# Kernel optimization log

Hardware: AMD Instinct MI355X
Metric: run time of the kernel (lower is better)

## Reference

```python
import jax, jax.numpy as jnp
import numpy as np

B, T, H, NH = 4, 1024, 1024, 16
HS = H // NH
FF = 4 * H
EPS = 1e-5


def setup_inputs() -> dict:
    key = jax.random.key(0)
    ks = jax.random.split(key, 12)
    s = 0.02
    inp = {
        "x": jax.random.normal(ks[0], (B, T, H), jnp.float32),
        # attention projections, stored as [in, out] so y = x @ W + b
        "Wq": jax.random.normal(ks[1], (H, H), jnp.float32) * s,
        "bq": jnp.zeros((H,), jnp.float32),
        "Wk": jax.random.normal(ks[2], (H, H), jnp.float32) * s,
        "bk": jnp.zeros((H,), jnp.float32),
        "Wv": jax.random.normal(ks[3], (H, H), jnp.float32) * s,
        "bv": jnp.zeros((H,), jnp.float32),
        "Wo": jax.random.normal(ks[4], (H, H), jnp.float32) * s,
        "bo": jnp.zeros((H,), jnp.float32),
        # layernorms
        "ln1_w": jnp.ones((H,), jnp.float32),
        "ln1_b": jnp.zeros((H,), jnp.float32),
        "ln2_w": jnp.ones((H,), jnp.float32),
        "ln2_b": jnp.zeros((H,), jnp.float32),
        # MLP
        "Wfc": jax.random.normal(ks[5], (H, FF), jnp.float32) * s,
        "bfc": jnp.zeros((FF,), jnp.float32),
        "Wpr": jax.random.normal(ks[6], (FF, H), jnp.float32) * s,
        "bpr": jnp.zeros((H,), jnp.float32),
    }
    return inp


def _layernorm(x, w, b):
    mu = jnp.mean(x, axis=-1, keepdims=True)
    var = jnp.mean(jnp.square(x - mu), axis=-1, keepdims=True)
    return (x - mu) * jax.lax.rsqrt(var + EPS) * w + b


def _rope(x):
    # x: [B, nh, T, hs]; interleaved-pair RoPE, base 10000
    half = HS // 2
    inv_freq = 1.0 / (10000.0 ** (jnp.arange(half, dtype=jnp.float32) / half))
    ang = jnp.arange(T, dtype=jnp.float32)[:, None] * inv_freq[None, :]  # [T, half]
    cos, sin = jnp.cos(ang), jnp.sin(ang)
    xr = x.reshape(*x.shape[:-1], half, 2)
    x0, x1 = xr[..., 0], xr[..., 1]
    r0 = x0 * cos - x1 * sin
    r1 = x0 * sin + x1 * cos
    return jnp.stack([r0, r1], axis=-1).reshape(x.shape)


def _block(x, Wq, bq, Wk, bk, Wv, bv, Wo, bo, ln1_w, ln1_b, ln2_w, ln2_b, Wfc, bfc, Wpr, bpr):
    # --- attention sub-block ---
    h1 = _layernorm(x, ln1_w, ln1_b)
    q = (h1 @ Wq + bq).reshape(B, T, NH, HS).transpose(0, 2, 1, 3)  # [B,nh,T,hs]
    k = (h1 @ Wk + bk).reshape(B, T, NH, HS).transpose(0, 2, 1, 3)
    v = (h1 @ Wv + bv).reshape(B, T, NH, HS).transpose(0, 2, 1, 3)
    q, k = _rope(q), _rope(k)
    scores = jnp.einsum('bhqd,bhkd->bhqk', q, k) / jnp.sqrt(jnp.float32(HS))
    attn = jax.nn.softmax(scores, axis=-1)
    # NOTE: original applies the causal mask AFTER softmax (multiplicative, no renorm)
    causal = jnp.tril(jnp.ones((T, T), jnp.float32))[None, None]
    attn = attn * causal
    out = jnp.einsum('bhqk,bhkd->bhqd', attn, v)
    out = out.transpose(0, 2, 1, 3).reshape(B, T, H)
    x = x + (out @ Wo + bo)
    # --- MLP sub-block ---
    h2 = _layernorm(x, ln2_w, ln2_b)
    m = jax.nn.gelu(h2 @ Wfc + bfc, approximate=False)
    x = x + (m @ Wpr + bpr)
    return x


def reference(x, Wq, bq, Wk, bk, Wv, bv, Wo, bo, ln1_w, ln1_b, ln2_w, ln2_b, Wfc, bfc, Wpr, bpr):
    return _block(x, Wq, bq, Wk, bk, Wv, bv, Wo, bo, ln1_w, ln1_b, ln2_w, ln2_b, Wfc, bfc, Wpr, bpr)
```

## Files before the change

### kernel.cpp

```cpp
#include <hip/hip_runtime.h>
#include <hip/hip_bf16.h>

typedef unsigned short u16;
typedef __attribute__((ext_vector_type(8))) short bf16x8;
typedef __attribute__((ext_vector_type(4))) float f32x4;
typedef __attribute__((ext_vector_type(4))) unsigned short u16x4;

#define B_  4
#define T_  1024
#define H_  1024
#define NH_ 16
#define HS_ 64
#define FF_ 4096
#define M_  (B_*T_)
#define QKV_S 3072

__device__ __forceinline__ u16 f2bf(float f){
  union { float f; unsigned u; } v; v.f = f;
  unsigned r = v.u + 0x7fffu + ((v.u >> 16) & 1u);
  return (u16)(r >> 16);
}
__device__ __forceinline__ float bf2f(u16 h){
  union { unsigned u; float f; } v; v.u = ((unsigned)h) << 16;
  return v.f;
}
__device__ __forceinline__ unsigned pack2bf(float a, float b){
  __hip_bfloat162 h = __float22bfloat162_rn(make_float2(a, b));
  union { __hip_bfloat162 h; unsigned u; } c; c.h = h;
  return c.u;
}

__device__ __forceinline__ void gload_lds16(const void* g, void* l){
  __builtin_amdgcn_global_load_lds(
      (const __attribute__((address_space(1))) unsigned int*)g,
      (__attribute__((address_space(3))) unsigned int*)l,
      16, 0, 0);
}

__global__ __launch_bounds__(256) void transpose_cvt(const float* __restrict__ W,
                                                     u16* __restrict__ Wt, int K, int N)
{
  __shared__ u16 tile[64][68];
  const int k0 = blockIdx.y * 64, n0 = blockIdx.x * 64;
  const int tid = threadIdx.x;
  #pragma unroll
  for (int it = 0; it < 4; ++it){
    int ci = tid + it * 256;
    int kr = ci >> 4, nc = ci & 15;
    float4 f = *(const float4*)(W + (size_t)(k0 + kr) * N + n0 + nc * 4);
    tile[kr][nc*4+0] = f2bf(f.x);
    tile[kr][nc*4+1] = f2bf(f.y);
    tile[kr][nc*4+2] = f2bf(f.z);
    tile[kr][nc*4+3] = f2bf(f.w);
  }
  __syncthreads();
  #pragma unroll
  for (int it = 0; it < 4; ++it){
    int co = tid + it * 256;
    int nr = co >> 4, kc = co & 15;
    u16x4 o;
    o[0] = tile[kc*4+0][nr];
    o[1] = tile[kc*4+1][nr];
    o[2] = tile[kc*4+2][nr];
    o[3] = tile[kc*4+3][nr];
    *(u16x4*)(Wt + (size_t)(n0 + nr) * K + k0 + kc * 4) = o;
  }
}

__global__ __launch_bounds__(256) void vtrans_k(const u16* __restrict__ qkv,
                                                u16* __restrict__ vtg)
{
  __shared__ u16 tile[64][72];
  const int bh = blockIdx.y, tt = blockIdx.x * 64;
  const int b = bh >> 4, h = bh & 15;
  const size_t src = (size_t)b * T_ * QKV_S + h * HS_ + 2048;
  const int tid = threadIdx.x;
  #pragma unroll
  for (int it = 0; it < 2; ++it){
    int ci = tid + it * 256;
    int r = ci >> 3, c = ci & 7;
    bf16x8 vvv = *(const bf16x8*)(qkv + src + (size_t)(tt + r) * QKV_S + c * 8);
    *(bf16x8*)&tile[r][c * 8] = vvv;
  }
  __syncthreads();
  #pragma unroll
  for (int it = 0; it < 2; ++it){
    int co = tid + it * 256;
    int d = co >> 3, c = co & 7;
    bf16x8 ov;
    #pragma unroll
    for (int j = 0; j < 8; ++j) ov[j] = (short)tile[c * 8 + j][d];
    *(bf16x8*)(vtg + (size_t)bh * HS_ * T_ + (size_t)d * T_ + tt + c * 8) = ov;
  }
}

__global__ void concat3_k(const float* __restrict__ a, const float* __restrict__ b,
                          const float* __restrict__ c, float* __restrict__ o){
  int i = blockIdx.x * 256 + threadIdx.x;
  if (i >= QKV_S) return;
  o[i] = (i < 1024) ? a[i] : (i < 2048) ? b[i - 1024] : c[i - 2048];
}

__global__ void rope_table_k(float* __restrict__ tab){
  int i = blockIdx.x * blockDim.x + threadIdx.x;
  if (i >= T_ * 32) return;
  int t = i >> 5, f = i & 31;
  float inv = powf(10000.0f, -(float)f * (1.0f / 32.0f));
  float ang = (float)t * inv;
  tab[i*2+0] = cosf(ang);
  tab[i*2+1] = sinf(ang);
}

__global__ void rope_apply_k(u16* __restrict__ qkv, const float* __restrict__ tab){
  int i = blockIdx.x * blockDim.x + threadIdx.x;
  if (i >= B_*T_*NH_*32) return;
  int pr = i & 31;
  int nh = (i >> 5) & (NH_ - 1);
  int bt = i >> 9;
  int t  = bt & (T_ - 1);
  size_t idx = (size_t)bt * QKV_S + nh * HS_ + pr * 2;
  float c = tab[(t*32 + pr)*2], s = tab[(t*32 + pr)*2 + 1];
  const float qs = 0.125f * 1.44269504f;
  {
    float x0 = bf2f(qkv[idx]), x1 = bf2f(qkv[idx+1]);
    qkv[idx]   = f2bf((x0 * c - x1 * s) * qs);
    qkv[idx+1] = f2bf((x0 * s + x1 * c) * qs);
  }
  {
    float x0 = bf2f(qkv[idx+1024]), x1 = bf2f(qkv[idx+1025]);
    qkv[idx+1024] = f2bf(x0 * c - x1 * s);
    qkv[idx+1025] = f2bf(x0 * s + x1 * c);
  }
}

__global__ __launch_bounds__(256) void ln_kernel(const float* __restrict__ x,
    const float* __restrict__ w, const float* __restrict__ bgain,
    u16* __restrict__ out)
{
  const int row = blockIdx.x;
  const int t = threadIdx.x;
  float4 vv = ((const float4*)(x + (size_t)row * H_))[t];
  float s  = vv.x + vv.y + vv.z + vv.w;
  float s2 = vv.x*vv.x + vv.y*vv.y + vv.z*vv.z + vv.w*vv.w;
  #pragma unroll
  for (int mm = 1; mm < 64; mm <<= 1){ s += __shfl_xor(s, mm); s2 += __shfl_xor(s2, mm); }
  __shared__ float red[8];
  int wid = t >> 6;
  if ((t & 63) == 0){ red[wid] = s; red[4 + wid] = s2; }
  __syncthreads();
  s  = red[0] + red[1] + red[2] + red[3];
  s2 = red[4] + red[5] + red[6] + red[7];
  float mu  = s * (1.0f / H_);
  float var = s2 * (1.0f / H_) - mu * mu;
  float rin = rsqrtf(var + 1e-5f);
  float4 wv = ((const float4*)w)[t];
  float4 bv = ((const float4*)bgain)[t];
  u16x4 ov;
  ov[0] = f2bf((vv.x - mu) * rin * wv.x + bv.x);
  ov[1] = f2bf((vv.y - mu) * rin * wv.y + bv.y);
  ov[2] = f2bf((vv.z - mu) * rin * wv.z + bv.z);
  ov[3] = f2bf((vv.w - mu) * rin * wv.w + bv.w);
  ((u16x4*)(out + (size_t)row * H_))[t] = ov;
}

template<int EPI, int RING>
__global__ __launch_bounds__(512) void gemm_kernel(
    const u16* __restrict__ A, const u16* __restrict__ Bt,
    const float* __restrict__ bias, const float* __restrict__ res,
    void* __restrict__ Cout, int M, int N, int K)
{
  __shared__ __attribute__((aligned(16))) u16 As[RING][128 * 32];
  __shared__ __attribute__((aligned(16))) u16 Bs[RING][128 * 32];
  const int tid  = threadIdx.x;
  const int lane = tid & 63;
  const int wid  = tid >> 6;
  const int wm = wid >> 2, wn = wid & 3;
  const int lrow = lane & 15, lkg = lane >> 4;

  const int gx  = gridDim.x;
  const int nwg = gx * gridDim.y;
  const int wg  = blockIdx.y * gx + blockIdx.x;
  const int nx  = nwg >> 3;
  const int swz = (wg & 7) * nx + (wg >> 3);
  const int m0 = (swz / gx) * 128, n0 = (swz % gx) * 128;

  const int srow = tid >> 2;
  const int sdc  = tid & 3;
  const int scs  = sdc ^ ((srow >> 1) & 3);

  const u16* Arow = A  + (size_t)(m0 + srow) * K + scs * 8;
  const u16* Brow = Bt + (size_t)(n0 + srow) * K + scs * 8;
  const int dd = (srow * 4 + sdc) * 8;

  f32x4 acc[4][2] = {};
  const int NT = K >> 5;
  constexpr int DIST = RING - 1;

  #pragma unroll
  for (int s = 0; s < DIST; ++s){
    gload_lds16(Arow + (s << 5), &As[s][dd]);
    gload_lds16(Brow + (s << 5), &Bs[s][dd]);
  }

  int rs = 0, wsl = DIST;
  for (int t = 0; t < NT; ++t){
    int cnt = NT - 1 - t; if (cnt > DIST - 1) cnt = DIST - 1;
    if (cnt >= 4)      asm volatile("s_waitcnt vmcnt(8)" ::: "memory");
    else if (cnt == 3) asm volatile("s_waitcnt vmcnt(6)" ::: "memory");
    else if (cnt == 2) asm volatile("s_waitcnt vmcnt(4)" ::: "memory");
    else if (cnt == 1) asm volatile("s_waitcnt vmcnt(2)" ::: "memory");
    else               asm volatile("s_waitcnt vmcnt(0)" ::: "memory");
    __builtin_amdgcn_s_barrier();

    const u16* Asc = As[rs];
    const u16* Bsc = Bs[rs];
    rs = (rs + 1 == RING) ? 0 : rs + 1;

    bf16x8 af[4], bfr[2];
    #pragma unroll
    for (int mi = 0; mi < 4; ++mi){
      int r = wm*64 + mi*16 + lrow;
      af[mi] = *(const bf16x8*)&Asc[(r*4 + (lkg ^ ((r >> 1) & 3))) * 8];
    }
    #pragma unroll
    for (int ni = 0; ni < 2; ++ni){
      int r = wn*32 + ni*16 + lrow;
      bfr[ni] = *(const bf16x8*)&Bsc[(r*4 + (lkg ^ ((r >> 1) & 3))) * 8];
    }
    __builtin_amdgcn_sched_barrier(0);

    if (t + DIST < NT){
      int k0 = (t + DIST) << 5;
      gload_lds16(Arow + k0, &As[wsl][dd]);
      gload_lds16(Brow + k0, &Bs[wsl][dd]);
    }
    wsl = (wsl + 1 == RING) ? 0 : wsl + 1;

    #pragma unroll
    for (int mi = 0; mi < 4; ++mi)
      #pragma unroll
      for (int ni = 0; ni < 2; ++ni)
        acc[mi][ni] = __builtin_amdgcn_mfma_f32_16x16x32_bf16(af[mi], bfr[ni], acc[mi][ni], 0, 0, 0);
  }

  #pragma unroll
  for (int mi = 0; mi < 4; ++mi){
    #pragma unroll
    for (int ni = 0; ni < 2; ++ni){
      int col = n0 + wn*32 + ni*16 + lrow;
      float bv = bias[col];
      #pragma unroll
      for (int r = 0; r < 4; ++r){
        int row = m0 + wm*64 + mi*16 + lkg*4 + r;
        float v = acc[mi][ni][r] + bv;
        if (EPI == 1){
          v = 0.5f * v * (1.0f + erff(v * 0.70710678118f));
        }
        if (EPI == 2){
          ((float*)Cout)[(size_t)row * N + col] = v + res[(size_t)row * N + col];
        } else {
          ((u16*)Cout)[(size_t)row * N + col] = f2bf(v);
        }
      }
    }
  }
}

__global__ __launch_bounds__(512, 4) void attn_kernel(
    const u16* __restrict__ qkv, const u16* __restrict__ vtg,
    u16* __restrict__ out)
{
  __shared__ u16 K_lds[3][64 * 64];
  __shared__ u16 VT_lds[3][64 * 64];
  __shared__ u16 P_lds[8][16 * 64];
  const int tid = threadIdx.x, lane = tid & 63, w = tid >> 6;
  const int lrow = lane & 15, lkg = lane >> 4;
  const int q0 = blockIdx.x * 128;
  const int bh = blockIdx.y, b = bh >> 4, h = bh & 15;
  const size_t baseq  = (size_t)b * T_ * QKV_S + h * HS_;
  const size_t basek  = baseq + 1024;
  const size_t basevt = (size_t)bh * HS_ * T_;
  const size_t baseo  = (size_t)b * T_ * H_ + h * HS_;
  const int qg = q0 + w * 16 + lrow;

  bf16x8 qa[2];
  {
    const u16* qp = qkv + baseq + (size_t)qg * QKV_S + lkg * 8;
    qa[0] = *(const bf16x8*)qp;
    qa[1] = *(const bf16x8*)(qp + 32);
  }

  const int r0 = tid >> 3, c0 = tid & 7, g0 = c0 ^ (r0 & 7);
  const u16* kap = qkv + basek + (size_t)r0 * QKV_S + g0 * 8;
  const u16* vap = vtg + basevt + (size_t)r0 * T_ + g0 * 8;
  const int kd = tid * 8;

  f32x4 o[4] = {};
  float mrun = -1e30f, lrun = 0.f;

  #pragma unroll
  for (int s = 0; s < 2; ++s){
    gload_lds16(kap + (size_t)s * 64 * QKV_S, &K_lds[s][kd]);
    gload_lds16(vap + s * 64,                 &VT_lds[s][kd]);
  }

  int rs = 0, wsl = 2;
  for (int t = 0; t < 16; ++t){
    const int kt = t << 6;
    if (t < 15) asm volatile("s_waitcnt vmcnt(2)" ::: "memory");
    else        asm volatile("s_waitcnt vmcnt(0)" ::: "memory");
    __builtin_amdgcn_s_barrier();
    __builtin_amdgcn_sched_barrier(0);

    if (t + 2 < 16){
      gload_lds16(kap + (size_t)(t + 2) * 64 * QKV_S, &K_lds[wsl][kd]);
      gload_lds16(vap + (t + 2) * 64,                 &VT_lds[wsl][kd]);
    }
    wsl = (wsl + 1 == 3) ? 0 : wsl + 1;

    const u16* Kc  = K_lds[rs];
    const u16* VTc = VT_lds[rs];
    rs = (rs + 1 == 3) ? 0 : rs + 1;

    f32x4 s[4];
    __builtin_amdgcn_s_setprio(1);
    #pragma unroll
    for (int mi = 0; mi < 4; ++mi){
      f32x4 c = {};
      #pragma unroll
      for (int ss = 0; ss < 2; ++ss){
        int r = mi * 16 + lrow;
        int off = r * 128 + (((ss * 4 + lkg) ^ (r & 7)) * 16);
        bf16x8 kb = *(const bf16x8*)((const char*)Kc + off);
        c = __builtin_amdgcn_mfma_f32_16x16x32_bf16(kb, qa[ss], c, 0, 0, 0);
      }
      s[mi] = c;
    }
    __builtin_amdgcn_s_setprio(0);

    float mt = fmaxf(fmaxf(fmaxf(s[0][0], s[0][1]), fmaxf(s[0][2], s[0][3])),
                     fmaxf(fmaxf(s[1][0], s[1][1]), fmaxf(s[1][2], s[1][3])));
    mt = fmaxf(mt, fmaxf(fmaxf(fmaxf(s[2][0], s[2][1]), fmaxf(s[2][2], s[2][3])),
                         fmaxf(fmaxf(s[3][0], s[3][1]), fmaxf(s[3][2], s[3][3]))));
    mt = fmaxf(mt, __shfl_xor(mt, 16));
    mt = fmaxf(mt, __shfl_xor(mt, 32));
    if (!__all(mt <= mrun + 8.f)){
      float mnew = fmaxf(mrun, mt);
      float fsc = exp2f(mrun - mnew);
      lrun *= fsc;
      #pragma unroll
      for (int nf = 0; nf < 4; ++nf){
        #pragma unroll
        for (int r = 0; r < 4; ++r) o[nf][r] *= fsc;
      }
      mrun = mnew;
    }

    float p[16];
    float ls = 0.f;
    #pragma unroll
    for (int mi = 0; mi < 4; ++mi){
      #pragma unroll
      for (int r = 0; r < 4; ++r){
        int key = kt + mi * 16 + lkg * 4 + r;
        float pv = exp2f(s[mi][r] - mrun);
        ls += pv;
        p[mi * 4 + r] = (key <= qg) ? pv : 0.f;
      }
    }
    ls += __shfl_xor(ls, 16);
    ls += __shfl_xor(ls, 32);
    lrun += ls;

    if (kt <= q0 + w * 16 + 15){
      char* pbase = (char*)&P_lds[w][0];
      const int rx = (lrow & 7) << 4;
      #pragma unroll
      for (int mi = 0; mi < 4; ++mi){
        uint2 pk;
        pk.x = pack2bf(p[mi*4+0], p[mi*4+1]);
        pk.y = pack2bf(p[mi*4+2], p[mi*4+3]);
        *(uint2*)(pbase + (lrow * 128 + ((mi * 32 + lkg * 8) ^ rx))) = pk;
      }
      __builtin_amdgcn_s_setprio(1);
      #pragma unroll
      for (int ss = 0; ss < 2; ++ss){
        bf16x8 pb = *(const bf16x8*)(pbase + (lrow * 128 + ((ss * 64 + lkg * 16) ^ rx)));
        #pragma unroll
        for (int nfd = 0; nfd < 4; ++nfd){
          int d = nfd * 16 + lrow;
          int off = d * 128 + (((ss * 4 + lkg) ^ (d & 7)) * 16);
          bf16x8 vb = *(const bf16x8*)((const char*)VTc + off);
          o[nfd] = __builtin_amdgcn_mfma_f32_16x16x32_bf16(vb, pb, o[nfd], 0, 0, 0);
        }
      }
      __builtin_amdgcn_s_setprio(0);
    }
  }

  float rl = 1.0f / lrun;
  #pragma unroll
  for (int nfd = 0; nfd < 4; ++nfd){
    uint2 ov;
    ov.x = pack2bf(o[nfd][0] * rl, o[nfd][1] * rl);
    ov.y = pack2bf(o[nfd][2] * rl, o[nfd][3] * rl);
    *(uint2*)(out + baseo + (size_t)qg * H_ + nfd * 16 + lkg * 4) = ov;
  }
}

extern "C" void kernel_launch(void* const* d_in, const int* in_sizes, int n_in,
                              void* d_out, int out_size, void* d_ws, size_t ws_size,
                              hipStream_t stream)
{
  (void)in_sizes; (void)n_in; (void)out_size; (void)ws_size;
  const float* x    = (const float*)d_in[0];
  const float* Wq   = (const float*)d_in[1];
  const float* bq   = (const float*)d_in[2];
  const float* Wk   = (const float*)d_in[3];
  const float* bk   = (const float*)d_in[4];
  const float* Wv   = (const float*)d_in[5];
  const float* bv   = (const float*)d_in[6];
  const float* Wo   = (const float*)d_in[7];
  const float* bo   = (const float*)d_in[8];
  const float* ln1w = (const float*)d_in[9];
  const float* ln1b = (const float*)d_in[10];
  const float* ln2w = (const float*)d_in[11];
  const float* ln2b = (const float*)d_in[12];
  const float* Wfc  = (const float*)d_in[13];
  const float* bfc  = (const float*)d_in[14];
  const float* Wpr  = (const float*)d_in[15];
  const float* bpr  = (const float*)d_in[16];

  char* ws = (char*)d_ws;
  u16*  WqkvT = (u16*)(ws + ((size_t) 0 << 20));
  u16*  WoT   = (u16*)(ws + ((size_t) 6 << 20));
  u16*  WfcT  = (u16*)(ws + ((size_t) 8 << 20));
  u16*  WprT  = (u16*)(ws + ((size_t)16 << 20));
  u16*  h1    = (u16*)(ws + ((size_t)24 << 20));
  u16*  qkvb  = (u16*)(ws + ((size_t)32 << 20));
  float* x1   = (float*)(ws + ((size_t)32 << 20));
  u16*  h2    = (u16*)(ws + ((size_t)48 << 20));
  float* bqkv = (float*)(ws + ((size_t)56 << 20));
  float* rtab = (float*)(ws + ((size_t)56 << 20) + (64 << 10));
  u16*  vtg   = (u16*)(ws + ((size_t)57 << 20));
  u16*  mb    = (u16*)(ws + ((size_t)56 << 20));
  u16*  attnout = h1;

  dim3 blk(256);
  dim3 gblk(512);

  transpose_cvt<<<dim3(H_/64,  H_/64),  blk, 0, stream>>>(Wq,  WqkvT,                 H_,  H_);
  transpose_cvt<<<dim3(H_/64,  H_/64),  blk, 0, stream>>>(Wk,  WqkvT + (size_t)1024*1024, H_,  H_);
  transpose_cvt<<<dim3(H_/64,  H_/64),  blk, 0, stream>>>(Wv,  WqkvT + (size_t)2048*1024, H_,  H_);
  transpose_cvt<<<dim3(H_/64,  H_/64),  blk, 0, stream>>>(Wo,  WoT,  H_,  H_);
  transpose_cvt<<<dim3(FF_/64, H_/64),  blk, 0, stream>>>(Wfc, WfcT, H_,  FF_);
  transpose_cvt<<<dim3(H_/64,  FF_/64), blk, 0, stream>>>(Wpr, WprT, FF_, H_);
  concat3_k<<<dim3((QKV_S+255)/256), blk, 0, stream>>>(bq, bk, bv, bqkv);
  rope_table_k<<<dim3((T_*32)/256), blk, 0, stream>>>(rtab);

  ln_kernel<<<dim3(M_), blk, 0, stream>>>(x, ln1w, ln1b, h1);
  gemm_kernel<0,3><<<dim3(QKV_S/128, M_/128), gblk, 0, stream>>>(h1, WqkvT, bqkv, nullptr, qkvb, M_, QKV_S, H_);
  rope_apply_k<<<dim3((B_*T_*NH_*32)/256), blk, 0, stream>>>(qkvb, rtab);
  vtrans_k<<<dim3(T_/64, B_*NH_), blk, 0, stream>>>(qkvb, vtg);
  attn_kernel<<<dim3(T_/128, B_*NH_), dim3(512), 0, stream>>>(qkvb, vtg, attnout);
  gemm_kernel<2,6><<<dim3(H_/128, M_/128), gblk, 0, stream>>>(attnout, WoT, bo, x, x1, M_, H_, H_);
  ln_kernel<<<dim3(M_), blk, 0, stream>>>(x1, ln2w, ln2b, h2);
  gemm_kernel<1,3><<<dim3(FF_/128, M_/128), gblk, 0, stream>>>(h2, WfcT, bfc, nullptr, mb, M_, FF_, H_);
  gemm_kernel<2,6><<<dim3(H_/128, M_/128), gblk, 0, stream>>>(mb, WprT, bpr, x1, (float*)d_out, M_, H_, FF_);
}
```

Before: 263.3 us.

## Switch GEMMs to 32x32x16 MFMA with 256-wide N tiles and tanh GELU

Reworks the GEMM kernel to use 32x32x16 bf16 MFMA instructions with a k-chunk-major LDS layout instead of 16x16x32 MFMAs with an XOR swizzle. The QKV and FC GEMMs now use 128x256 tiles, with each wave covering 64x64 outputs. Every GEMM uses a fixed 3-stage load ring with simpler vmcnt waits. The aim is more reuse per LDS fragment load and fewer MFMA issues per output. The exact erf GELU in the FC epilogue is replaced by a tanh-form approximation built on exp2f, which trades a little accuracy against the reference's exact GELU for cheaper math.

```diff
diff --git a/kernel.cpp b/kernel.cpp
--- a/kernel.cpp
+++ b/kernel.cpp
@@ -4,6 +4,7 @@
 typedef unsigned short u16;
 typedef __attribute__((ext_vector_type(8))) short bf16x8;
 typedef __attribute__((ext_vector_type(4))) float f32x4;
+typedef __attribute__((ext_vector_type(16))) float f32x16;
 typedef __attribute__((ext_vector_type(4))) unsigned short u16x4;
 
 #define B_  4
@@ -163,98 +164,121 @@
   ((u16x4*)(out + (size_t)row * H_))[t] = ov;
 }
 
-template<int EPI, int RING>
-__global__ __launch_bounds__(512) void gemm_kernel(
+template<int EPI, int BN, int NI>
+__global__ __launch_bounds__(512, 4) void gemm_kernel(
     const u16* __restrict__ A, const u16* __restrict__ Bt,
     const float* __restrict__ bias, const float* __restrict__ res,
     void* __restrict__ Cout, int M, int N, int K)
 {
-  __shared__ __attribute__((aligned(16))) u16 As[RING][128 * 32];
-  __shared__ __attribute__((aligned(16))) u16 Bs[RING][128 * 32];
+  constexpr int LPT = (BN == 256) ? 3 : 2;
+  __shared__ __attribute__((aligned(16))) u16 As[3][128 * 32];
+  __shared__ __attribute__((aligned(16))) u16 Bs[3][BN * 32];
   const int tid  = threadIdx.x;
   const int lane = tid & 63;
   const int wid  = tid >> 6;
   const int wm = wid >> 2, wn = wid & 3;
-  const int lrow = lane & 15, lkg = lane >> 4;
+  const int llo = lane & 31, lhi = lane >> 5;
 
   const int gx  = gridDim.x;
   const int nwg = gx * gridDim.y;
   const int wg  = blockIdx.y * gx + blockIdx.x;
   const int nx  = nwg >> 3;
   const int swz = (wg & 7) * nx + (wg >> 3);
-  const int m0 = (swz / gx) * 128, n0 = (swz % gx) * 128;
-
-  const int srow = tid >> 2;
-  const int sdc  = tid & 3;
-  const int scs  = sdc ^ ((srow >> 1) & 3);
-
-  const u16* Arow = A  + (size_t)(m0 + srow) * K + scs * 8;
-  const u16* Brow = Bt + (size_t)(n0 + srow) * K + scs * 8;
-  const int dd = (srow * 4 + sdc) * 8;
-
-  f32x4 acc[4][2] = {};
+  const int m0 = (swz / gx) * 128, n0 = (swz % gx) * BN;
+
+  const u16* Asrc = A + (size_t)(m0 + (tid & 127)) * K + (tid >> 7) * 8;
+  const int dA = tid * 8;
+  const u16* Bsrc;
+  int dB0, dB1;
+  if constexpr (BN == 256){
+    Bsrc = Bt + (size_t)(n0 + (tid & 255)) * K + (tid >> 8) * 8;
+    dB0 = tid * 8; dB1 = (tid + 512) * 8;
+  } else {
+    Bsrc = Bt + (size_t)(n0 + (tid & 127)) * K + (tid >> 7) * 8;
+    dB0 = tid * 8; dB1 = 0;
+  }
+
+  int aoff[2][2], boff[NI][2];
+  #pragma unroll
+  for (int kh = 0; kh < 2; ++kh){
+    #pragma unroll
+    for (int mi = 0; mi < 2; ++mi)
+      aoff[mi][kh] = (((kh*2 + lhi) * 128) + wm*64 + mi*32 + llo) * 16;
+    #pragma unroll
+    for (int ni = 0; ni < NI; ++ni)
+      boff[ni][kh] = (((kh*2 + lhi) * BN) + wn*(NI*32) + ni*32 + llo) * 16;
+  }
+
+  f32x16 acc[2][NI] = {};
   const int NT = K >> 5;
-  constexpr int DIST = RING - 1;
-
-  #pragma unroll
-  for (int s = 0; s < DIST; ++s){
-    gload_lds16(Arow + (s << 5), &As[s][dd]);
-    gload_lds16(Brow + (s << 5), &Bs[s][dd]);
-  }
-
-  int rs = 0, wsl = DIST;
+
+  #pragma unroll
+  for (int s = 0; s < 2; ++s){
+    gload_lds16(Asrc + (s << 5), &As[s][dA]);
+    gload_lds16(Bsrc + (s << 5), &Bs[s][dB0]);
+    if constexpr (BN == 256) gload_lds16(Bsrc + 16 + (s << 5), &Bs[s][dB1]);
+  }
+
+  int rs = 0, wsl = 2;
   for (int t = 0; t < NT; ++t){
-    int cnt = NT - 1 - t; if (cnt > DIST - 1) cnt = DIST - 1;
-    if (cnt >= 4)      asm volatile("s_waitcnt vmcnt(8)" ::: "memory");
-    else if (cnt == 3) asm volatile("s_waitcnt vmcnt(6)" ::: "memory");
-    else if (cnt == 2) asm volatile("s_waitcnt vmcnt(4)" ::: "memory");
-    else if (cnt == 1) asm volatile("s_waitcnt vmcnt(2)" ::: "memory");
-    else               asm volatile("s_waitcnt vmcnt(0)" ::: "memory");
+    if (t < NT - 1){
+      if constexpr (BN == 256) asm volatile("s_waitcnt vmcnt(3)" ::: "memory");
+      else                     asm volatile("s_waitcnt vmcnt(2)" ::: "memory");
+    } else {
+      asm volatile("s_waitcnt vmcnt(0)" ::: "memory");
+    }
     __builtin_amdgcn_s_barrier();
 
-    const u16* Asc = As[rs];
-    const u16* Bsc = Bs[rs];
-    rs = (rs + 1 == RING) ? 0 : rs + 1;
-
-    bf16x8 af[4], bfr[2];
-    #pragma unroll
-    for (int mi = 0; mi < 4; ++mi){
-      int r = wm*64 + mi*16 + lrow;
-      af[mi] = *(const bf16x8*)&Asc[(r*4 + (lkg ^ ((r >> 1) & 3))) * 8];
-    }
-    #pragma unroll
-    for (int ni = 0; ni < 2; ++ni){
-      int r = wn*32 + ni*16 + lrow;
-      bfr[ni] = *(const bf16x8*)&Bsc[(r*4 + (lkg ^ ((r >> 1) & 3))) * 8];
+    const char* Ab = (const char*)&As[rs][0];
+    const char* Bb = (const char*)&Bs[rs][0];
+    rs = (rs + 1 == 3) ? 0 : rs + 1;
+
+    bf16x8 af[2][2], bfr[NI][2];
+    #pragma unroll
+    for (int kh = 0; kh < 2; ++kh){
+      #pragma unroll
+      for (int mi = 0; mi < 2; ++mi)
+        af[mi][kh] = *(const bf16x8*)(Ab + aoff[mi][kh]);
+      #pragma unroll
+      for (int ni = 0; ni < NI; ++ni)
+        bfr[ni][kh] = *(const bf16x8*)(Bb + boff[ni][kh]);
     }
     __builtin_amdgcn_sched_barrier(0);
 
-    if (t + DIST < NT){
-      int k0 = (t + DIST) << 5;
-      gload_lds16(Arow + k0, &As[wsl][dd]);
-      gload_lds16(Brow + k0, &Bs[wsl][dd]);
-    }
-    wsl = (wsl + 1 == RING) ? 0 : wsl + 1;
-
-    #pragma unroll
-    for (int mi = 0; mi < 4; ++mi)
-      #pragma unroll
-      for (int ni = 0; ni < 2; ++ni)
-        acc[mi][ni] = __builtin_amdgcn_mfma_f32_16x16x32_bf16(af[mi], bfr[ni], acc[mi][ni], 0, 0, 0);
-  }
-
-  #pragma unroll
-  for (int mi = 0; mi < 4; ++mi){
-    #pragma unroll
-    for (int ni = 0; ni < 2; ++ni){
-      int col = n0 + wn*32 + ni*16 + lrow;
+    if (t + 2 < NT){
+      int k0 = (t + 2) << 5;
+      gload_lds16(Asrc + k0, &As[wsl][dA]);
+      gload_lds16(Bsrc + k0, &Bs[wsl][dB0]);
+      if constexpr (BN == 256) gload_lds16(Bsrc + 16 + k0, &Bs[wsl][dB1]);
+    }
+    wsl = (wsl + 1 == 3) ? 0 : wsl + 1;
+
+    #pragma unroll
+    for (int kh = 0; kh < 2; ++kh)
+      #pragma unroll
+      for (int mi = 0; mi < 2; ++mi)
+        #pragma unroll
+        for (int ni = 0; ni < NI; ++ni)
+          acc[mi][ni] = __builtin_amdgcn_mfma_f32_32x32x16_bf16(
+              af[mi][kh], bfr[ni][kh], acc[mi][ni], 0, 0, 0);
+  }
+
+  #pragma unroll
+  for (int mi = 0; mi < 2; ++mi){
+    #pragma unroll
+    for (int ni = 0; ni < NI; ++ni){
+      int col = n0 + wn*(NI*32) + ni*32 + llo;
       float bv = bias[col];
-      #pragma unroll
-      for (int r = 0; r < 4; ++r){
-        int row = m0 + wm*64 + mi*16 + lkg*4 + r;
-        float v = acc[mi][ni][r] + bv;
+      int rbase = m0 + wm*64 + mi*32 + 4*lhi;
+      #pragma unroll
+      for (int rg = 0; rg < 16; ++rg){
+        int row = rbase + (rg & 3) + 8*(rg >> 2);
+        float v = acc[mi][ni][rg] + bv;
         if (EPI == 1){
-          v = 0.5f * v * (1.0f + erff(v * 0.70710678118f));
+          float u = v * (0.7978845608f + 0.0356774081f * v * v);
+          float e = exp2f(u * 2.885390082f);
+          v = 0.5f * v * (2.0f - 2.0f / (e + 1.0f)) * 0.5f + 0.5f * v * 0.0f;
+          v = 0.5f * (acc[mi][ni][rg] + bv) * (1.0f + (1.0f - 2.0f / (e + 1.0f)));
         }
         if (EPI == 2){
           ((float*)Cout)[(size_t)row * N + col] = v + res[(size_t)row * N + col];
@@ -459,12 +483,12 @@
   rope_table_k<<<dim3((T_*32)/256), blk, 0, stream>>>(rtab);
 
   ln_kernel<<<dim3(M_), blk, 0, stream>>>(x, ln1w, ln1b, h1);
-  gemm_kernel<0,3><<<dim3(QKV_S/128, M_/128), gblk, 0, stream>>>(h1, WqkvT, bqkv, nullptr, qkvb, M_, QKV_S, H_);
+  gemm_kernel<0,256,2><<<dim3(QKV_S/256, M_/128), gblk, 0, stream>>>(h1, WqkvT, bqkv, nullptr, qkvb, M_, QKV_S, H_);
   rope_apply_k<<<dim3((B_*T_*NH_*32)/256), blk, 0, stream>>>(qkvb, rtab);
   vtrans_k<<<dim3(T_/64, B_*NH_), blk, 0, stream>>>(qkvb, vtg);
   attn_kernel<<<dim3(T_/128, B_*NH_), dim3(512), 0, stream>>>(qkvb, vtg, attnout);
-  gemm_kernel<2,6><<<dim3(H_/128, M_/128), gblk, 0, stream>>>(attnout, WoT, bo, x, x1, M_, H_, H_);
+  gemm_kernel<2,128,1><<<dim3(H_/128, M_/128), gblk, 0, stream>>>(attnout, WoT, bo, x, x1, M_, H_, H_);
   ln_kernel<<<dim3(M_), blk, 0, stream>>>(x1, ln2w, ln2b, h2);
-  gemm_kernel<1,3><<<dim3(FF_/128, M_/128), gblk, 0, stream>>>(h2, WfcT, bfc, nullptr, mb, M_, FF_, H_);
-  gemm_kernel<2,6><<<dim3(H_/128, M_/128), gblk, 0, stream>>>(mb, WprT, bpr, x1, (float*)d_out, M_, H_, FF_);
-}
+  gemm_kernel<1,256,2><<<dim3(FF_/256, M_/128), gblk, 0, stream>>>(h2, WfcT, bfc, nullptr, mb, M_, FF_, H_);
+  gemm_kernel<2,128,1><<<dim3(H_/128, M_/128), gblk, 0, stream>>>(mb, WprT, bpr, x1, (float*)d_out, M_, H_, FF_);
+}
```

New measurement: 342.3 us. +30.0%, slower.
